# Kernel tuning notes

Measured on AMD Instinct MI355X. Metric: run time of the kernel, lower is better.

Reference implementation:

```python
import jax, jax.numpy as jnp
import numpy as np

N_NODES = 100000
N_EDGES = 1600000
N_HIDDEN = 128
EPS = 1e-12  # F.normalize default eps


def setup_inputs() -> dict:
    key = jax.random.key(0)
    k1, k2, k3, k4 = jax.random.split(key, 4)
    emb = jax.random.normal(k1, (N_NODES, N_HIDDEN), dtype=jnp.float32)
    d = jnp.ones((N_HIDDEN,), dtype=jnp.float32)          # nn.Parameter ones
    scale = jnp.full((1,), 0.5, dtype=jnp.float32)        # nn.Parameter 0.5
    src = jax.random.randint(k2, (N_EDGES,), 0, N_NODES)
    dst = jax.random.randint(k3, (N_EDGES,), 0, N_NODES)
    return {"emb": emb, "d": d, "scale": scale, "src": src, "dst": dst}


def reference(emb, d, scale, src, dst):
    # L2 normalize rows (torch F.normalize: x / max(||x||, eps))
    norm = jnp.sqrt(jnp.sum(emb * emb, axis=1, keepdims=True))
    e = emb / jnp.maximum(norm, EPS)            # [N, H]
    ew = e * d                                   # emb @ diag(d), as elementwise scale
    # u_dot_v: per-edge dot product of src 'ew' and dst 'e' -> [E, 1]
    z = jnp.sum(ew[src] * e[dst], axis=-1, keepdims=True)
    return z * scale
```

## Files before the change

kernel.cpp:

```cpp
#include <hip/hip_runtime.h>

#define HIDDEN 128
#define EPS 1e-12f

__device__ __forceinline__ int pack4(float x, float y, float z, float w, float s) {
    int q0 = (int)rintf(x * s);
    int q1 = (int)rintf(y * s);
    int q2 = (int)rintf(z * s);
    int q3 = (int)rintf(w * s);
    return (q0 & 255) | ((q1 & 255) << 8) | ((q2 & 255) << 16) | (q3 << 24);
}

__device__ __forceinline__ int dot4i8(int a, int b, int c) {
#if __has_builtin(__builtin_amdgcn_sdot4)
    return __builtin_amdgcn_sdot4(a, b, c, false);
#else
    int r = c;
    r += ((a << 24) >> 24) * ((b << 24) >> 24);
    r += ((a << 16) >> 24) * ((b << 16) >> 24);
    r += ((a <<  8) >> 24) * ((b <<  8) >> 24);
    r += (a >> 24) * (b >> 24);
    return r;
#endif
}

__global__ __launch_bounds__(256) void normalize_quant_kernel(
    const float* __restrict__ emb, const float* __restrict__ d,
    int* __restrict__ ewq, int* __restrict__ eq,
    float* __restrict__ s_ew, float* __restrict__ s_e, int n_nodes) {
    int row  = blockIdx.x * 8 + (threadIdx.x >> 5);
    if (row >= n_nodes) return;
    int lane = threadIdx.x & 31;

    float4 v = ((const float4*)emb)[(size_t)row * 32 + lane];
    float ss = v.x * v.x + v.y * v.y + v.z * v.z + v.w * v.w;
    #pragma unroll
    for (int m = 16; m >= 1; m >>= 1) ss += __shfl_xor(ss, m);
    float inv = 1.0f / fmaxf(sqrtf(ss), EPS);

    float4 e4, w4;
    float4 d4 = ((const float4*)d)[lane];
    e4.x = v.x * inv; e4.y = v.y * inv; e4.z = v.z * inv; e4.w = v.w * inv;
    w4.x = e4.x * d4.x; w4.y = e4.y * d4.y; w4.z = e4.z * d4.z; w4.w = e4.w * d4.w;

    float me = fmaxf(fmaxf(fabsf(e4.x), fabsf(e4.y)), fmaxf(fabsf(e4.z), fabsf(e4.w)));
    float mw = fmaxf(fmaxf(fabsf(w4.x), fabsf(w4.y)), fmaxf(fabsf(w4.z), fabsf(w4.w)));
    #pragma unroll
    for (int m = 16; m >= 1; m >>= 1) {
        me = fmaxf(me, __shfl_xor(me, m));
        mw = fmaxf(mw, __shfl_xor(mw, m));
    }

    float inv_e = me > 0.0f ? 127.0f / me : 0.0f;
    float inv_w = mw > 0.0f ? 127.0f / mw : 0.0f;

    eq [(size_t)row * 32 + lane] = pack4(e4.x, e4.y, e4.z, e4.w, inv_e);
    ewq[(size_t)row * 32 + lane] = pack4(w4.x, w4.y, w4.z, w4.w, inv_w);
    if (lane == 0) {
        s_e [row] = me * (1.0f / 127.0f);
        s_ew[row] = mw * (1.0f / 127.0f);
    }
}

__global__ __launch_bounds__(256) void edge_dot_kernel(
    const int* __restrict__ ewq, const int* __restrict__ eq,
    const float* __restrict__ s_ew, const float* __restrict__ s_e,
    const float* __restrict__ scale, const int* __restrict__ src,
    const int* __restrict__ dst, float* __restrict__ out, int n_edges) {
    int group = blockIdx.x * 32 + (threadIdx.x >> 3);
    int lane  = threadIdx.x & 7;
    int base  = group * 4;
    if (base >= n_edges) return;

    int s[4], t[4];
    if (base + 3 < n_edges) {
        int4 s4 = ((const int4*)src)[group];
        int4 t4 = ((const int4*)dst)[group];
        s[0] = s4.x; s[1] = s4.y; s[2] = s4.z; s[3] = s4.w;
        t[0] = t4.x; t[1] = t4.y; t[2] = t4.z; t[3] = t4.w;
    } else {
        #pragma unroll
        for (int j = 0; j < 4; ++j) {
            int e = min(base + j, n_edges - 1);
            s[j] = src[e]; t[j] = dst[e];
        }
    }

    int4 a[4], b[4];
    #pragma unroll
    for (int j = 0; j < 4; ++j) {
        a[j] = ((const int4*)ewq)[(size_t)s[j] * 8 + lane];
        b[j] = ((const int4*)eq )[(size_t)t[j] * 8 + lane];
    }

    float r0 = 0.0f; int ss = 0, tt = 0;
    #pragma unroll
    for (int j = 0; j < 4; ++j) {
        int acc = 0;
        acc = dot4i8(a[j].x, b[j].x, acc);
        acc = dot4i8(a[j].y, b[j].y, acc);
        acc = dot4i8(a[j].z, b[j].z, acc);
        acc = dot4i8(a[j].w, b[j].w, acc);
        #pragma unroll
        for (int m = 4; m >= 1; m >>= 1) acc += __shfl_xor(acc, m);
        if (lane == j) { r0 = (float)acc; ss = s[j]; tt = t[j]; }
    }

    int e = base + lane;
    if (lane < 4 && e < n_edges)
        out[e] = r0 * s_ew[ss] * s_e[tt] * scale[0];
}

extern "C" void kernel_launch(void* const* d_in, const int* in_sizes, int n_in,
                              void* d_out, int out_size, void* d_ws, size_t ws_size,
                              hipStream_t stream) {
    const float* emb   = (const float*)d_in[0];
    const float* d     = (const float*)d_in[1];
    const float* scale = (const float*)d_in[2];
    const int*   src   = (const int*)d_in[3];
    const int*   dst   = (const int*)d_in[4];
    float*       out   = (float*)d_out;

    int n_nodes = in_sizes[0] / HIDDEN;
    int n_edges = in_sizes[3];

    int*   ewq  = (int*)d_ws;
    int*   eq   = ewq + (size_t)n_nodes * 32;
    float* s_ew = (float*)(eq + (size_t)n_nodes * 32);
    float* s_e  = s_ew + n_nodes;

    int blocks1 = (n_nodes + 7) / 8;
    normalize_quant_kernel<<<blocks1, 256, 0, stream>>>(emb, d, ewq, eq, s_ew, s_e, n_nodes);

    int blocks2 = (n_edges + 127) / 128;
    edge_dot_kernel<<<blocks2, 256, 0, stream>>>(ewq, eq, s_ew, s_e, scale, src, dst, out, n_edges);
}
```

Before: 154.8 us.

## Store one shared sqrt(|d|)-scaled int8 table and apply d's sign via masked dots

Splits the diagonal weight d symmetrically as sqrt(|d|) on both sides, so source and destination can share a single quantized table and per-row scale instead of two. The sign of d is kept in a byte mask, and each dot product is computed as a masked positive part minus a masked negative part. This halves the quantization write in the first kernel and the gather footprint for cache reuse in the edge kernel. The cost is twice as many sdot4 operations plus mask logic per edge, and a different quantization error profile.

```diff
diff --git a/kernel.cpp b/kernel.cpp
--- a/kernel.cpp
+++ b/kernel.cpp
@@ -26,8 +26,18 @@
 
 __global__ __launch_bounds__(256) void normalize_quant_kernel(
     const float* __restrict__ emb, const float* __restrict__ d,
-    int* __restrict__ ewq, int* __restrict__ eq,
-    float* __restrict__ s_ew, float* __restrict__ s_e, int n_nodes) {
+    int* __restrict__ q, float* __restrict__ sf, int* __restrict__ mp,
+    int n_nodes) {
+    if (blockIdx.x == 0 && threadIdx.x < 32) {
+        const float* dd = d + threadIdx.x * 4;
+        int m = 0;
+        if (dd[0] >= 0.0f) m |= 0x000000FF;
+        if (dd[1] >= 0.0f) m |= 0x0000FF00;
+        if (dd[2] >= 0.0f) m |= 0x00FF0000;
+        if (dd[3] >= 0.0f) m |= 0xFF000000;
+        mp[threadIdx.x] = m;
+    }
+
     int row  = blockIdx.x * 8 + (threadIdx.x >> 5);
     if (row >= n_nodes) return;
     int lane = threadIdx.x & 31;
@@ -38,39 +48,37 @@
     for (int m = 16; m >= 1; m >>= 1) ss += __shfl_xor(ss, m);
     float inv = 1.0f / fmaxf(sqrtf(ss), EPS);
 
-    float4 e4, w4;
     float4 d4 = ((const float4*)d)[lane];
-    e4.x = v.x * inv; e4.y = v.y * inv; e4.z = v.z * inv; e4.w = v.w * inv;
-    w4.x = e4.x * d4.x; w4.y = e4.y * d4.y; w4.z = e4.z * d4.z; w4.w = e4.w * d4.w;
+    float4 f4;
+    f4.x = sqrtf(fabsf(d4.x)); f4.y = sqrtf(fabsf(d4.y));
+    f4.z = sqrtf(fabsf(d4.z)); f4.w = sqrtf(fabsf(d4.w));
 
-    float me = fmaxf(fmaxf(fabsf(e4.x), fabsf(e4.y)), fmaxf(fabsf(e4.z), fabsf(e4.w)));
+    float4 w4;
+    w4.x = v.x * inv * f4.x; w4.y = v.y * inv * f4.y;
+    w4.z = v.z * inv * f4.z; w4.w = v.w * inv * f4.w;
+
     float mw = fmaxf(fmaxf(fabsf(w4.x), fabsf(w4.y)), fmaxf(fabsf(w4.z), fabsf(w4.w)));
     #pragma unroll
-    for (int m = 16; m >= 1; m >>= 1) {
-        me = fmaxf(me, __shfl_xor(me, m));
-        mw = fmaxf(mw, __shfl_xor(mw, m));
-    }
+    for (int m = 16; m >= 1; m >>= 1) mw = fmaxf(mw, __shfl_xor(mw, m));
 
-    float inv_e = me > 0.0f ? 127.0f / me : 0.0f;
     float inv_w = mw > 0.0f ? 127.0f / mw : 0.0f;
-
-    eq [(size_t)row * 32 + lane] = pack4(e4.x, e4.y, e4.z, e4.w, inv_e);
-    ewq[(size_t)row * 32 + lane] = pack4(w4.x, w4.y, w4.z, w4.w, inv_w);
-    if (lane == 0) {
-        s_e [row] = me * (1.0f / 127.0f);
-        s_ew[row] = mw * (1.0f / 127.0f);
-    }
+    q[(size_t)row * 32 + lane] = pack4(w4.x, w4.y, w4.z, w4.w, inv_w);
+    if (lane == 0) sf[row] = mw * (1.0f / 127.0f);
 }
 
 __global__ __launch_bounds__(256) void edge_dot_kernel(
-    const int* __restrict__ ewq, const int* __restrict__ eq,
-    const float* __restrict__ s_ew, const float* __restrict__ s_e,
+    const int* __restrict__ q, const float* __restrict__ sf,
     const float* __restrict__ scale, const int* __restrict__ src,
-    const int* __restrict__ dst, float* __restrict__ out, int n_edges) {
+    const int* __restrict__ dst, const int* __restrict__ mp,
+    float* __restrict__ out, int n_edges) {
     int group = blockIdx.x * 32 + (threadIdx.x >> 3);
     int lane  = threadIdx.x & 7;
     int base  = group * 4;
     if (base >= n_edges) return;
+
+    int4 maskp = ((const int4*)mp)[lane];
+    int4 maskn;
+    maskn.x = ~maskp.x; maskn.y = ~maskp.y; maskn.z = ~maskp.z; maskn.w = ~maskp.w;
 
     int s[4], t[4];
     if (base + 3 < n_edges) {
@@ -89,18 +97,23 @@
     int4 a[4], b[4];
     #pragma unroll
     for (int j = 0; j < 4; ++j) {
-        a[j] = ((const int4*)ewq)[(size_t)s[j] * 8 + lane];
-        b[j] = ((const int4*)eq )[(size_t)t[j] * 8 + lane];
+        a[j] = ((const int4*)q)[(size_t)s[j] * 8 + lane];
+        b[j] = ((const int4*)q)[(size_t)t[j] * 8 + lane];
     }
 
     float r0 = 0.0f; int ss = 0, tt = 0;
     #pragma unroll
     for (int j = 0; j < 4; ++j) {
-        int acc = 0;
-        acc = dot4i8(a[j].x, b[j].x, acc);
-        acc = dot4i8(a[j].y, b[j].y, acc);
-        acc = dot4i8(a[j].z, b[j].z, acc);
-        acc = dot4i8(a[j].w, b[j].w, acc);
+        int p = 0, n = 0;
+        p = dot4i8(a[j].x & maskp.x, b[j].x, p);
+        n = dot4i8(a[j].x & maskn.x, b[j].x, n);
+        p = dot4i8(a[j].y & maskp.y, b[j].y, p);
+        n = dot4i8(a[j].y & maskn.y, b[j].y, n);
+        p = dot4i8(a[j].z & maskp.z, b[j].z, p);
+        n = dot4i8(a[j].z & maskn.z, b[j].z, n);
+        p = dot4i8(a[j].w & maskp.w, b[j].w, p);
+        n = dot4i8(a[j].w & maskn.w, b[j].w, n);
+        int acc = p - n;
         #pragma unroll
         for (int m = 4; m >= 1; m >>= 1) acc += __shfl_xor(acc, m);
         if (lane == j) { r0 = (float)acc; ss = s[j]; tt = t[j]; }
@@ -108,7 +121,7 @@
 
     int e = base + lane;
     if (lane < 4 && e < n_edges)
-        out[e] = r0 * s_ew[ss] * s_e[tt] * scale[0];
+        out[e] = r0 * sf[ss] * sf[tt] * scale[0];
 }
 
 extern "C" void kernel_launch(void* const* d_in, const int* in_sizes, int n_in,
@@ -124,14 +137,13 @@
     int n_nodes = in_sizes[0] / HIDDEN;
     int n_edges = in_sizes[3];
 
-    int*   ewq  = (int*)d_ws;
-    int*   eq   = ewq + (size_t)n_nodes * 32;
-    float* s_ew = (float*)(eq + (size_t)n_nodes * 32);
-    float* s_e  = s_ew + n_nodes;
+    int*   q  = (int*)d_ws;
+    float* sf = (float*)(q + (size_t)n_nodes * 32);
+    int*   mp = (int*)(sf + n_nodes);
 
     int blocks1 = (n_nodes + 7) / 8;
-    normalize_quant_kernel<<<blocks1, 256, 0, stream>>>(emb, d, ewq, eq, s_ew, s_e, n_nodes);
+    normalize_quant_kernel<<<blocks1, 256, 0, stream>>>(emb, d, q, sf, mp, n_nodes);
 
     int blocks2 = (n_edges + 127) / 128;
-    edge_dot_kernel<<<blocks2, 256, 0, stream>>>(ewq, eq, s_ew, s_e, scale, src, dst, out, n_edges);
+    edge_dot_kernel<<<blocks2, 256, 0, stream>>>(q, sf, scale, src, dst, mp, out, n_edges);
 }
```

Result: faster. 146.9 us (-5.1%).
